# Performance work log

Measured on AMD Instinct MI355X. Metric: run time of the kernel, lower is better.

## Reference

```python
import jax, jax.numpy as jnp
import numpy as np

N_NODES = 100000
N_EDGES = 1600000
D_IN = 64
D_OUT = 64


def setup_inputs() -> dict:
    key = jax.random.key(0)
    k1, k2, k3, k4, k5, k6 = jax.random.split(key, 6)
    x = jax.random.normal(k1, (N_NODES, D_IN), dtype=jnp.float32)
    weight = jax.random.normal(k2, (D_IN, D_OUT), dtype=jnp.float32) * (1.0 / np.sqrt(D_OUT))
    bias = jax.random.normal(k3, (D_OUT,), dtype=jnp.float32) * (1.0 / np.sqrt(D_OUT))
    adj_vals = jax.random.uniform(k4, (N_EDGES,), dtype=jnp.float32)
    src = jax.random.randint(k5, (N_EDGES,), 0, N_NODES, dtype=jnp.int32)
    dst = jax.random.randint(k6, (N_EDGES,), 0, N_NODES, dtype=jnp.int32)
    return {"x": x, "weight": weight, "bias": bias, "adj_vals": adj_vals, "src": src, "dst": dst}


def reference(x, weight, bias, adj_vals, src, dst):
    # support = X @ W  -> [N, D_OUT]
    support = jnp.dot(x, weight)
    # sparse adjacency matmul: out[dst] += adj_vals * support[src]
    msgs = adj_vals[:, None] * support[src]  # [E, D_OUT]
    out = jax.ops.segment_sum(msgs, dst, num_segments=N_NODES)
    return out + bias
```

## Files before the change

kernel.cpp:

```cpp
#include <hip/hip_runtime.h>

#define N_NODES 100000
#define N_EDGES 1600000
#define D 64

#define BN 64
#define NBUCK ((N_NODES + BN - 1) / BN)
#define CHW 512
#define CH ((N_EDGES + CHW - 1) / CHW)
#define CITER 7
#define CAP 2048
#define SMAX 2048
#define PAD 16
#define OVFMAX 32768
#define GEMM_THREADS (N_NODES * 16 / 2)
#define GEMM_BLKS ((GEMM_THREADS + 511) / 512)
#define NBLK (CHW + GEMM_BLKS)

static __device__ __forceinline__ unsigned short f2bf(float f) {
    unsigned u = __float_as_uint(f);
    u += 0x7FFFu + ((u >> 16) & 1u);
    return (unsigned short)(u >> 16);
}
static __device__ __forceinline__ float bf2f(unsigned short h) {
    return __uint_as_float((unsigned)h << 16);
}

__global__ __launch_bounds__(512, 4) void gcn_main(const float* __restrict__ x,
                                                   const float* __restrict__ w,
                                                   unsigned short* __restrict__ support,
                                                   const int* __restrict__ src,
                                                   const int* __restrict__ dst,
                                                   const float* __restrict__ adj,
                                                   int* __restrict__ gcur,
                                                   int* __restrict__ ovfcnt,
                                                   int4* __restrict__ ovflist,
                                                   int2* __restrict__ coarse) {
    __shared__ __align__(16) char smem[16384];
    int tid = threadIdx.x;
    int bid = blockIdx.x;

    if (bid < CHW) {
        int* h = (int*)smem;
        int* cur = h + NBUCK;
        for (int i = tid; i < NBUCK; i += 512) h[i] = 0;
        __syncthreads();

        int e0 = bid * CH, e1 = min(e0 + CH, N_EDGES);
        int dreg[CITER], sreg[CITER];
        float areg[CITER];
        #pragma unroll
        for (int it = 0; it < CITER; ++it) {
            int e = e0 + tid + it * 512;
            dreg[it] = -1;
            if (e < e1) {
                dreg[it] = __builtin_nontemporal_load(&dst[e]);
                sreg[it] = __builtin_nontemporal_load(&src[e]);
                areg[it] = __builtin_nontemporal_load(&adj[e]);
                atomicAdd(&h[dreg[it] >> 6], 1);
            }
        }
        __syncthreads();

        for (int c = tid; c < NBUCK; c += 512) {
            int hc = h[c];
            if (hc) cur[c] = atomicAdd(&gcur[c * PAD], hc);
        }
        __syncthreads();

        #pragma unroll
        for (int it = 0; it < CITER; ++it) {
            if (dreg[it] >= 0) {
                int c = dreg[it] >> 6;
                int pos = atomicAdd(&cur[c], 1);
                if (pos < CAP) {
                    coarse[c * CAP + pos] =
                        make_int2(sreg[it] | ((dreg[it] & 63) << 17),
                                  __float_as_int(areg[it]));
                } else {
                    int op = atomicAdd(ovfcnt, 1);
                    if (op < OVFMAX)
                        ovflist[op] = make_int4(sreg[it], dreg[it],
                                                __float_as_int(areg[it]), 0);
                }
            }
        }
    } else {
        float4* wsh = (float4*)smem;
        const float4* w4 = (const float4*)w;
        for (int i = tid; i < 64 * 16; i += 512) wsh[i] = w4[i];
        __syncthreads();

        int idx = (bid - CHW) * 512 + tid;
        if (idx < GEMM_THREADS) {
            int rowpair = idx >> 4;
            int c4 = idx & 15;
            long r0 = (long)rowpair * 2;
            const float4* xr0 = (const float4*)(x + r0 * D);
            const float4* xr1 = (const float4*)(x + (r0 + 1) * D);

            float4 a0 = make_float4(0.f, 0.f, 0.f, 0.f);
            float4 a1 = make_float4(0.f, 0.f, 0.f, 0.f);
            #pragma unroll 4
            for (int k4 = 0; k4 < 16; ++k4) {
                float4 xv0 = xr0[k4];
                float4 xv1 = xr1[k4];
                float4 w0 = wsh[(4 * k4 + 0) * 16 + c4];
                float4 w1 = wsh[(4 * k4 + 1) * 16 + c4];
                float4 w2 = wsh[(4 * k4 + 2) * 16 + c4];
                float4 w3 = wsh[(4 * k4 + 3) * 16 + c4];
                a0 += w0 * xv0.x + w1 * xv0.y + w2 * xv0.z + w3 * xv0.w;
                a1 += w0 * xv1.x + w1 * xv1.y + w2 * xv1.z + w3 * xv1.w;
            }
            ushort4* s4 = (ushort4*)support;
            s4[r0 * 16 + c4] = make_ushort4(f2bf(a0.x), f2bf(a0.y), f2bf(a0.z), f2bf(a0.w));
            s4[(r0 + 1) * 16 + c4] = make_ushort4(f2bf(a1.x), f2bf(a1.y), f2bf(a1.z), f2bf(a1.w));
        }
    }
}

__global__ __launch_bounds__(256) void gcn_bgather(const unsigned short* __restrict__ support,
                                                   const int2* __restrict__ coarse,
                                                   const int* __restrict__ gcur,
                                                   const int* __restrict__ ovfcnt,
                                                   const int4* __restrict__ ovflist,
                                                   const float* __restrict__ bias,
                                                   float* __restrict__ out) {
    __shared__ int2 sE[SMAX];
    __shared__ int cntS[BN], loffS[BN], curS[BN];

    int tid = threadIdx.x, wv = tid >> 6, lane = tid & 63;
    int b = blockIdx.x;
    int tot = min(gcur[b * PAD], CAP);
    const int2* ce = coarse + (long)b * CAP;

    if (tid < BN) cntS[tid] = 0;
    __syncthreads();

    for (int e = tid; e < tot; e += 256)
        atomicAdd(&cntS[(ce[e].x >> 17) & 63], 1);
    __syncthreads();

    if (tid < BN) loffS[tid] = cntS[tid];
    __syncthreads();
    for (int off = 1; off < BN; off <<= 1) {
        int t = 0;
        if (tid < BN && tid >= off) t = loffS[tid - off];
        __syncthreads();
        if (tid < BN && tid >= off) loffS[tid] += t;
        __syncthreads();
    }
    if (tid < BN) {
        int excl = loffS[tid] - cntS[tid];
        loffS[tid] = excl;
        curS[tid] = excl;
    }
    __syncthreads();

    for (int e = tid; e < tot; e += 256) {
        int2 ed = ce[e];
        int nl = (ed.x >> 17) & 63;
        int pos = atomicAdd(&curS[nl], 1);
        sE[pos] = ed;
    }
    __syncthreads();

    int eg = lane >> 4;
    int L  = lane & 15;
    const uint2* sup2 = (const uint2*)support;
    const float4* bias4 = (const float4*)bias;
    float4* out4 = (float4*)out;
    float4 bv = bias4[L];

    for (int nl = wv * 16; nl < wv * 16 + 16; ++nl) {
        int start = loffS[nl];
        int avail = cntS[nl];
        float4 acc = make_float4(0.f, 0.f, 0.f, 0.f);
        #pragma unroll 2
        for (int j = 0; j < avail; j += 16) {
            #pragma unroll
            for (int q = 0; q < 4; ++q) {
                int ei = j + q * 4 + eg;
                int2 ed = sE[start + min(ei, avail - 1)];
                float wgt = (ei < avail) ? __int_as_float(ed.y) : 0.f;
                uint2 p = sup2[(long)(ed.x & 0x1FFFF) * 16 + L];
                acc.x += wgt * __uint_as_float(p.x << 16);
                acc.y += wgt * __uint_as_float(p.x & 0xFFFF0000u);
                acc.z += wgt * __uint_as_float(p.y << 16);
                acc.w += wgt * __uint_as_float(p.y & 0xFFFF0000u);
            }
        }
        acc.x += __shfl_xor(acc.x, 16, 64); acc.y += __shfl_xor(acc.y, 16, 64);
        acc.z += __shfl_xor(acc.z, 16, 64); acc.w += __shfl_xor(acc.w, 16, 64);
        acc.x += __shfl_xor(acc.x, 32, 64); acc.y += __shfl_xor(acc.y, 32, 64);
        acc.z += __shfl_xor(acc.z, 32, 64); acc.w += __shfl_xor(acc.w, 32, 64);
        int n = b * BN + nl;
        if (lane < 16 && n < N_NODES) {
            float4 r = make_float4(acc.x + bv.x, acc.y + bv.y,
                                   acc.z + bv.z, acc.w + bv.w);
            out4[(long)n * 16 + L] = r;
        }
    }

    __syncthreads();
    int no = min(*ovfcnt, OVFMAX);
    for (int i = wv; i < no; i += 4) {
        int4 ed = ovflist[i];
        if ((ed.y >> 6) == b) {
            float v = __int_as_float(ed.z) * bf2f(support[(long)ed.x * D + lane]);
            atomicAdd(&out[(long)ed.y * D + lane], v);
        }
    }
}

extern "C" void kernel_launch(void* const* d_in, const int* in_sizes, int n_in,
                              void* d_out, int out_size, void* d_ws, size_t ws_size,
                              hipStream_t stream) {
    const float* x      = (const float*)d_in[0];
    const float* weight = (const float*)d_in[1];
    const float* bias   = (const float*)d_in[2];
    const float* adj    = (const float*)d_in[3];
    const int*   src    = (const int*)d_in[4];
    const int*   dst    = (const int*)d_in[5];
    float* out = (float*)d_out;

    unsigned short* support = (unsigned short*)d_ws;
    int2* coarse = (int2*)(support + (long)N_NODES * D);
    int*  gcur   = (int*)(coarse + (long)NBUCK * CAP);
    int*  ovfcnt = gcur + NBUCK * PAD;
    int4* ovflist = (int4*)(ovfcnt + 4);

    hipMemsetAsync(gcur, 0, NBUCK * PAD * sizeof(int) + 16, stream);
    hipLaunchKernelGGL(gcn_main, dim3(NBLK), dim3(512), 0, stream,
                       x, weight, support, src, dst, adj, gcur, ovfcnt, ovflist, coarse);
    hipLaunchKernelGGL(gcn_bgather, dim3(NBUCK), dim3(256), 0, stream,
                       support, coarse, gcur, ovfcnt, ovflist, bias, out);
}
```

Before: 191.5 us.

## Replace per-bucket counting sort with shared-memory atomic accumulation in gather

The gather kernel no longer counting-sorts each bucket's edges by local node through histogram, scan and scatter passes. Each 16-lane group now takes an edge, loads the bf16 support row and atomically adds the weighted values into a padded shared-memory accumulator per node, then writes the result plus bias. This removes several barriers and scan passes but adds LDS float atomics that contend when edges hit the same node. The binning phase also uses half as many chunk blocks, each handling more edges, and drops the occupancy hint from launch bounds.

Measured after the change: 731.0 us. 282% more time.

```diff
diff --git a/kernel.cpp b/kernel.cpp
--- a/kernel.cpp
+++ b/kernel.cpp
@@ -6,16 +6,16 @@
 
 #define BN 64
 #define NBUCK ((N_NODES + BN - 1) / BN)
-#define CHW 512
+#define CHW 256
 #define CH ((N_EDGES + CHW - 1) / CHW)
-#define CITER 7
+#define CITER 13
 #define CAP 2048
-#define SMAX 2048
 #define PAD 16
 #define OVFMAX 32768
 #define GEMM_THREADS (N_NODES * 16 / 2)
 #define GEMM_BLKS ((GEMM_THREADS + 511) / 512)
 #define NBLK (CHW + GEMM_BLKS)
+#define STR 68
 
 static __device__ __forceinline__ unsigned short f2bf(float f) {
     unsigned u = __float_as_uint(f);
@@ -26,16 +26,16 @@
     return __uint_as_float((unsigned)h << 16);
 }
 
-__global__ __launch_bounds__(512, 4) void gcn_main(const float* __restrict__ x,
-                                                   const float* __restrict__ w,
-                                                   unsigned short* __restrict__ support,
-                                                   const int* __restrict__ src,
-                                                   const int* __restrict__ dst,
-                                                   const float* __restrict__ adj,
-                                                   int* __restrict__ gcur,
-                                                   int* __restrict__ ovfcnt,
-                                                   int4* __restrict__ ovflist,
-                                                   int2* __restrict__ coarse) {
+__global__ __launch_bounds__(512) void gcn_main(const float* __restrict__ x,
+                                                const float* __restrict__ w,
+                                                unsigned short* __restrict__ support,
+                                                const int* __restrict__ src,
+                                                const int* __restrict__ dst,
+                                                const float* __restrict__ adj,
+                                                int* __restrict__ gcur,
+                                                int* __restrict__ ovfcnt,
+                                                int4* __restrict__ ovflist,
+                                                int2* __restrict__ coarse) {
     __shared__ __align__(16) char smem[16384];
     int tid = threadIdx.x;
     int bid = blockIdx.x;
@@ -126,83 +126,49 @@
                                                    const int4* __restrict__ ovflist,
                                                    const float* __restrict__ bias,
                                                    float* __restrict__ out) {
-    __shared__ int2 sE[SMAX];
-    __shared__ int cntS[BN], loffS[BN], curS[BN];
-
-    int tid = threadIdx.x, wv = tid >> 6, lane = tid & 63;
+    __shared__ float accS[BN * STR];
+
+    int tid = threadIdx.x;
     int b = blockIdx.x;
     int tot = min(gcur[b * PAD], CAP);
     const int2* ce = coarse + (long)b * CAP;
 
-    if (tid < BN) cntS[tid] = 0;
+    for (int i = tid; i < BN * STR; i += 256) accS[i] = 0.f;
     __syncthreads();
 
-    for (int e = tid; e < tot; e += 256)
-        atomicAdd(&cntS[(ce[e].x >> 17) & 63], 1);
-    __syncthreads();
-
-    if (tid < BN) loffS[tid] = cntS[tid];
-    __syncthreads();
-    for (int off = 1; off < BN; off <<= 1) {
-        int t = 0;
-        if (tid < BN && tid >= off) t = loffS[tid - off];
-        __syncthreads();
-        if (tid < BN && tid >= off) loffS[tid] += t;
-        __syncthreads();
-    }
-    if (tid < BN) {
-        int excl = loffS[tid] - cntS[tid];
-        loffS[tid] = excl;
-        curS[tid] = excl;
-    }
-    __syncthreads();
-
-    for (int e = tid; e < tot; e += 256) {
+    int g = tid >> 4;
+    int L = tid & 15;
+    const uint2* sup2 = (const uint2*)support;
+
+    #pragma unroll 4
+    for (int e = g; e < tot; e += 16) {
         int2 ed = ce[e];
         int nl = (ed.x >> 17) & 63;
-        int pos = atomicAdd(&curS[nl], 1);
-        sE[pos] = ed;
+        float wgt = __int_as_float(ed.y);
+        uint2 p = sup2[(long)(ed.x & 0x1FFFF) * 16 + L];
+        float* a = &accS[nl * STR + L * 4];
+        atomicAdd(&a[0], wgt * __uint_as_float(p.x << 16));
+        atomicAdd(&a[1], wgt * __uint_as_float(p.x & 0xFFFF0000u));
+        atomicAdd(&a[2], wgt * __uint_as_float(p.y << 16));
+        atomicAdd(&a[3], wgt * __uint_as_float(p.y & 0xFFFF0000u));
     }
     __syncthreads();
 
-    int eg = lane >> 4;
-    int L  = lane & 15;
-    const uint2* sup2 = (const uint2*)support;
     const float4* bias4 = (const float4*)bias;
     float4* out4 = (float4*)out;
-    float4 bv = bias4[L];
-
-    for (int nl = wv * 16; nl < wv * 16 + 16; ++nl) {
-        int start = loffS[nl];
-        int avail = cntS[nl];
-        float4 acc = make_float4(0.f, 0.f, 0.f, 0.f);
-        #pragma unroll 2
-        for (int j = 0; j < avail; j += 16) {
-            #pragma unroll
-            for (int q = 0; q < 4; ++q) {
-                int ei = j + q * 4 + eg;
-                int2 ed = sE[start + min(ei, avail - 1)];
-                float wgt = (ei < avail) ? __int_as_float(ed.y) : 0.f;
-                uint2 p = sup2[(long)(ed.x & 0x1FFFF) * 16 + L];
-                acc.x += wgt * __uint_as_float(p.x << 16);
-                acc.y += wgt * __uint_as_float(p.x & 0xFFFF0000u);
-                acc.z += wgt * __uint_as_float(p.y << 16);
-                acc.w += wgt * __uint_as_float(p.y & 0xFFFF0000u);
-            }
-        }
-        acc.x += __shfl_xor(acc.x, 16, 64); acc.y += __shfl_xor(acc.y, 16, 64);
-        acc.z += __shfl_xor(acc.z, 16, 64); acc.w += __shfl_xor(acc.w, 16, 64);
-        acc.x += __shfl_xor(acc.x, 32, 64); acc.y += __shfl_xor(acc.y, 32, 64);
-        acc.z += __shfl_xor(acc.z, 32, 64); acc.w += __shfl_xor(acc.w, 32, 64);
+    for (int i = tid; i < BN * 16; i += 256) {
+        int nl = i >> 4, q = i & 15;
         int n = b * BN + nl;
-        if (lane < 16 && n < N_NODES) {
-            float4 r = make_float4(acc.x + bv.x, acc.y + bv.y,
-                                   acc.z + bv.z, acc.w + bv.w);
-            out4[(long)n * 16 + L] = r;
+        if (n < N_NODES) {
+            float4 bv = bias4[q];
+            const float* a = &accS[nl * STR + q * 4];
+            out4[(long)n * 16 + q] = make_float4(a[0] + bv.x, a[1] + bv.y,
+                                                 a[2] + bv.z, a[3] + bv.w);
         }
     }
 
     __syncthreads();
+    int lane = tid & 63, wv = tid >> 6;
     int no = min(*ovfcnt, OVFMAX);
     for (int i = wv; i < no; i += 4) {
         int4 ed = ovflist[i];
```
